# Optimization experiments

Measured on AMD Instinct MI355X. Metric: run time of the kernel, lower is better.

The kernel has to match this reference:

```python
import jax, jax.numpy as jnp
import numpy as np
from jax import lax

# --- constructor constants (init_kwargs) ---
NMS_THRESH = 0.0
NMS_KSIZE = 5
TOP_K = 512
GAUSS_KSIZE = 15
GAUSS_SIGMA = 0.5
LOSS_LAMBDA = 100.0
BORDER = 8  # border width zeroed by filter_border (RF-Net convention)

B, C, H, W = 8, 1, 512, 640


def setup_inputs() -> dict:
    key = jax.random.key(0)
    k1, k2, k3 = jax.random.split(key, 3)
    score1 = jax.random.uniform(k1, (B, C, H, W), dtype=jnp.float32)
    score2 = jax.random.uniform(k2, (B, C, H, W), dtype=jnp.float32)
    # near-identity homographies: small affine perturbation + few-pixel translation
    scale = jnp.array([[0.02, 0.02, 5.0], [0.02, 0.02, 5.0], [1e-5, 1e-5, 0.0]], jnp.float32)
    homo12 = jnp.eye(3, dtype=jnp.float32)[None] + jax.random.normal(k3, (B, 3, 3), jnp.float32) * scale[None]
    return {"score1": score1, "score2": score2, "homo12": homo12}


def filter_border(x, pad=BORDER):
    m = jnp.zeros((x.shape[-2], x.shape[-1]), x.dtype).at[pad:-pad, pad:-pad].set(1.0)
    return x * m


def warp_image(img, homo):
    # Sample img (frame 2) at homo @ p1 for every pixel p1; zero outside. img: B,C,H,W
    b, c, h, w = img.shape
    ys, xs = jnp.meshgrid(jnp.arange(h, dtype=jnp.float32), jnp.arange(w, dtype=jnp.float32), indexing="ij")
    p1 = jnp.stack([xs, ys, jnp.ones_like(xs)], 0).reshape(3, -1)
    p2 = jnp.einsum("bij,jn->bin", homo, p1)
    x2 = (p2[:, 0] / p2[:, 2]).reshape(b, h, w)
    y2 = (p2[:, 1] / p2[:, 2]).reshape(b, h, w)

    x0 = jnp.floor(x2); y0 = jnp.floor(y2)
    x1 = x0 + 1.0; y1 = y0 + 1.0
    wa = (x1 - x2) * (y1 - y2); wb = (x2 - x0) * (y1 - y2)
    wc = (x1 - x2) * (y2 - y0); wd = (x2 - x0) * (y2 - y0)

    bidx = jnp.arange(b)[:, None, None]

    def gather(yc, xc):
        valid = (xc >= 0) & (xc <= w - 1) & (yc >= 0) & (yc <= h - 1)
        xi = jnp.clip(xc, 0, w - 1).astype(jnp.int32)
        yi = jnp.clip(yc, 0, h - 1).astype(jnp.int32)
        g = img[bidx, :, yi, xi]  # B,H,W,C
        return g * valid[..., None].astype(img.dtype)

    out = (wa[..., None] * gather(y0, x0) + wb[..., None] * gather(y0, x1)
           + wc[..., None] * gather(y1, x0) + wd[..., None] * gather(y1, x1))
    return jnp.transpose(out, (0, 3, 1, 2))


def nms(score):
    # zero-pad (matches F.pad + max_pool2d), local-max + threshold mask
    pad = NMS_KSIZE // 2
    p = jnp.pad(score, ((0, 0), (0, 0), (pad, pad), (pad, pad)))
    fmax = lax.reduce_window(p, -jnp.inf, lax.max, (1, 1, NMS_KSIZE, NMS_KSIZE), (1, 1, 1, 1), "VALID")
    mask = (score > NMS_THRESH) & (score == fmax)
    return score * mask.astype(score.dtype)


def select_score_and_keypoints(score):
    s = nms(score)
    b, c, h, w = s.shape
    flat = s.reshape(b * c, h * w)
    vals, idx = lax.top_k(flat, TOP_K)
    sel = jnp.zeros_like(flat).at[jnp.arange(b * c)[:, None], idx].set(vals)
    sel = sel.reshape(b, c, h, w)
    kp = jnp.stack([idx // w, idx % w], -1).reshape(b, c, TOP_K, 2)  # (y, x)
    return sel, kp


def gaussian_filter(x):
    r = GAUSS_KSIZE // 2
    ax = jnp.arange(-r, r + 1, dtype=jnp.float32)
    g1 = jnp.exp(-(ax ** 2) / (2.0 * GAUSS_SIGMA ** 2))
    kern = jnp.outer(g1, g1)  # unnormalized (peak = 1), RF-Net style
    c = x.shape[1]
    k = jnp.broadcast_to(kern[None, None], (c, 1, GAUSS_KSIZE, GAUSS_KSIZE))
    return lax.conv_general_dilated(x, k, (1, 1), "SAME", feature_group_count=c)


def reference(score1, score2, homo12):
    w_score2 = warp_image(score2, homo12)
    s1 = filter_border(score1)
    w2 = filter_border(w_score2)
    w_vis_mask = (warp_image(jnp.ones_like(score2), homo12) > 0).astype(s1.dtype)
    _, kp1 = select_score_and_keypoints(s1)
    gt_score1, _ = select_score_and_keypoints(w2)
    gt_score1 = gaussian_filter(gt_score1)
    norm = w_vis_mask.sum()
    loss = (((s1 - gt_score1) ** 2) * w_vis_mask / norm).sum() * LOSS_LAMBDA
    return loss, kp1
```

## Files before the change

kernel.cpp:

```cpp
#include <hip/hip_runtime.h>

#define NB 8
#define NH 512
#define NW 640
#define NHW (NH*NW)
#define TOPK 512
#define PAD 8
#define NBIN2 256
#define GCAP 4096
#define NTILE 160
#define TSLOT 256

#define TW 64
#define TH 32
#define INH 36
#define INW 72

#define G0 1.0f
#define G1 0.1353352832366127f
#define G2 3.3546262790251185e-4f

#define M_TCNT 0
#define M_THIST 2560
#define M_DENSE 657920
#define M_WCNT 660480
#define M_ACCUM 660488
#define M_DCNT 660496
#define M_WINNERS 660504
#define M_END (M_WINNERS + 8192)

__device__ __forceinline__ float bordered(const float* __restrict__ img, int b, int y, int x) {
  if (y < PAD || y >= NH - PAD || x < PAD || x >= NW - PAD) return 0.f;
  return img[b * NHW + y * NW + x];
}

__device__ __forceinline__ int vbin(float val) {
  int d = 0x3F800000 - (int)__float_as_uint(val);
  if (d < 0) d = 0;
  unsigned int bk = (unsigned int)d >> 14;
  return bk > (NBIN2 - 1) ? (NBIN2 - 1) : (int)bk;
}

__device__ __forceinline__ void corner(const float* __restrict__ img, float cx, float cy,
                                       float wgt, float& acc) {
  float valid = (cx >= 0.f && cx <= (float)(NW - 1) && cy >= 0.f && cy <= (float)(NH - 1)) ? 1.f : 0.f;
  float xc = fminf(fmaxf(cx, 0.f), (float)(NW - 1));
  float yc = fminf(fmaxf(cy, 0.f), (float)(NH - 1));
  int xi = (int)xc, yi = (int)yc;
  acc += wgt * img[yi * NW + xi] * valid;
}

__device__ __forceinline__ float vis_quad(float h0, float h1, float h2, float h3, float h4,
                                          float h5, float h6, float h7, float h8,
                                          float xf, float yf) {
  float X = h0 * xf + h1 * yf + h2;
  float Y = h3 * xf + h4 * yf + h5;
  float Z = h6 * xf + h7 * yf + h8;
  bool ok = ((X + Z) * Z > 0.f) & ((640.f * Z - X) * Z > 0.f)
          & ((Y + Z) * Z > 0.f) & ((512.f * Z - Y) * Z > 0.f);
  return ok ? 1.f : 0.f;
}

__device__ __forceinline__ void vis_parts(float h0, float h1, float h2, float h3, float h4,
                                          float h5, float h6, float h7, float h8,
                                          float xf, float yf, float L[5]) {
  float X = h0 * xf + h1 * yf + h2;
  float Y = h3 * xf + h4 * yf + h5;
  float Z = h6 * xf + h7 * yf + h8;
  L[0] = X + Z; L[1] = 640.f * Z - X; L[2] = Y + Z; L[3] = 512.f * Z - Y; L[4] = Z;
}

__global__ __launch_bounds__(256) void k_nms5(
    const float* __restrict__ score1, const float* __restrict__ score2,
    const float* __restrict__ homo,
    unsigned long long* __restrict__ lists, unsigned int* __restrict__ meta) {
  int bx = blockIdx.x, by = blockIdx.y, b = blockIdx.z;
  int tid = threadIdx.x;
  int t = by * 10 + bx;

  __shared__ float in[INH][INW];
  __shared__ float hmax[INH][TW];
  __shared__ unsigned int s_cnt;
  __shared__ unsigned int s_bh[NBIN2];
  __shared__ float s_wsum[4];
  __shared__ unsigned int s_wcnt[4];

  const float* hm = homo + b * 9;
  float h0 = hm[0], h1 = hm[1], h2 = hm[2];
  float h3 = hm[3], h4 = hm[4], h5 = hm[5];
  float h6 = hm[6], h7 = hm[7], h8 = hm[8];

  int y0t = by * TH, x0t = bx * TW;

  for (int src = 0; src < 2; ++src) {
    if (tid == 0) s_cnt = 0;
    s_bh[tid] = 0;

    if (src == 0) {
      #pragma unroll
      for (int it = 0; it < 3; ++it) {
        int i = it * 256 + tid;
        if (i < INH * 18) {
          int r = i / 18, c4 = i % 18;
          int gy = y0t + r - 2;
          int gx0 = x0t - 4 + c4 * 4;
          float4 v = make_float4(0.f, 0.f, 0.f, 0.f);
          if (gy >= PAD && gy < NH - PAD) {
            const float4* p = (const float4*)(score1 + (size_t)b * NHW + (size_t)gy * NW + gx0);
            float4 raw = *p;
            v.x = (gx0 + 0 >= PAD && gx0 + 0 < NW - PAD) ? raw.x : 0.f;
            v.y = (gx0 + 1 >= PAD && gx0 + 1 < NW - PAD) ? raw.y : 0.f;
            v.z = (gx0 + 2 >= PAD && gx0 + 2 < NW - PAD) ? raw.z : 0.f;
            v.w = (gx0 + 3 >= PAD && gx0 + 3 < NW - PAD) ? raw.w : 0.f;
          }
          *(float4*)&in[r][c4 * 4] = v;
        }
      }
    } else {
      const float* img = score2 + b * NHW;
      #pragma unroll
      for (int it = 0; it < 10; ++it) {
        int i = it * 256 + tid;
        if (i < INH * 68) {
          int r = i / 68, c = i % 68;
          int gy = y0t + r - 2, gx = x0t - 2 + c;
          float v = 0.f;
          if (gy >= PAD && gy < NH - PAD && gx >= PAD && gx < NW - PAD) {
            float xf = (float)gx, yf = (float)gy;
            float X = h0 * xf + h1 * yf + h2;
            float Y = h3 * xf + h4 * yf + h5;
            float Z = h6 * xf + h7 * yf + h8;
            float rz = __builtin_amdgcn_rcpf(Z);
            float x2 = X * rz, y2 = Y * rz;
            float x0f = floorf(x2), y0f = floorf(y2);
            float x1f = x0f + 1.f, y1f = y0f + 1.f;
            float wa = (x1f - x2) * (y1f - y2);
            float wb = (x2 - x0f) * (y1f - y2);
            float wc = (x1f - x2) * (y2 - y0f);
            float wd = (x2 - x0f) * (y2 - y0f);
            float acc = 0.f;
            if (x0f >= 0.f && x1f <= 639.f && y0f >= 0.f && y1f <= 511.f) {
              const float* p = img + (int)y0f * NW + (int)x0f;
              acc = fmaf(wa, p[0], acc);
              acc = fmaf(wb, p[1], acc);
              acc = fmaf(wc, p[NW], acc);
              acc = fmaf(wd, p[NW + 1], acc);
            } else {
              corner(img, x0f, y0f, wa, acc);
              corner(img, x1f, y0f, wb, acc);
              corner(img, x0f, y1f, wc, acc);
              corner(img, x1f, y1f, wd, acc);
            }
            v = acc;
          }
          in[r][c + 2] = v;
        }
      }
    }
    __syncthreads();

    #pragma unroll
    for (int it = 0; it < 9; ++it) {
      int i = it * 256 + tid;
      int r = i >> 6, c = i & 63;
      float m = fmaxf(fmaxf(fmaxf(in[r][c + 2], in[r][c + 3]), fmaxf(in[r][c + 4], in[r][c + 5])),
                      in[r][c + 6]);
      hmax[r][c] = m;
    }
    __syncthreads();

    bool uni = false;
    float vconst = 0.f;
    if (src == 0) {
      float c00[5], c10[5], c01[5], c11[5];
      vis_parts(h0, h1, h2, h3, h4, h5, h6, h7, h8, (float)x0t, (float)y0t, c00);
      vis_parts(h0, h1, h2, h3, h4, h5, h6, h7, h8, (float)(x0t + TW - 1), (float)y0t, c10);
      vis_parts(h0, h1, h2, h3, h4, h5, h6, h7, h8, (float)x0t, (float)(y0t + TH - 1), c01);
      vis_parts(h0, h1, h2, h3, h4, h5, h6, h7, h8, (float)(x0t + TW - 1), (float)(y0t + TH - 1), c11);
      uni = true;
      bool sig[5];
      #pragma unroll
      for (int q = 0; q < 5; ++q) {
        bool allp = (c00[q] > 0.f) & (c10[q] > 0.f) & (c01[q] > 0.f) & (c11[q] > 0.f);
        bool alln = (c00[q] < 0.f) & (c10[q] < 0.f) & (c01[q] < 0.f) & (c11[q] < 0.f);
        uni = uni & (allp | alln);
        sig[q] = allp;
      }
      vconst = (sig[0] == sig[4] && sig[1] == sig[4] && sig[2] == sig[4] && sig[3] == sig[4])
               ? 1.f : 0.f;
    }

    int nsv = 0;
    float sv[8];
    unsigned int si[8];
    float tsum = 0.f;
    int vcnt = 0;
    #pragma unroll
    for (int it = 0; it < (TH * TW) / 256; ++it) {
      int i = it * 256 + tid;
      int r = i >> 6, c = i & 63;
      int gy = y0t + r, gx = x0t + c;
      float val = in[r + 2][c + 4];
      if (src == 0) {
        float v = uni ? vconst
                      : vis_quad(h0, h1, h2, h3, h4, h5, h6, h7, h8, (float)gx, (float)gy);
        tsum += val * val * v;
        vcnt += (v > 0.f) ? 1 : 0;
      }
      if (val > 0.f) {
        float m = fmaxf(fmaxf(fmaxf(hmax[r][c], hmax[r + 1][c]), fmaxf(hmax[r + 2][c], hmax[r + 3][c])),
                        hmax[r + 4][c]);
        if (m == val) {
          sv[nsv] = val;
          si[nsv] = (unsigned int)(gy * NW + gx);
          ++nsv;
        }
      }
    }

    unsigned int local = 0;
    if (nsv > 0) local = atomicAdd(&s_cnt, (unsigned int)nsv);
    #pragma unroll
    for (int j = 0; j < 8; ++j)
      if (j < nsv) atomicAdd(&s_bh[vbin(sv[j])], 1u);

    if (src == 0) {
      for (int m = 1; m < 64; m <<= 1) {
        tsum += __shfl_xor(tsum, m, 64);
        vcnt += __shfl_xor(vcnt, m, 64);
      }
      if ((tid & 63) == 0) { s_wsum[tid >> 6] = tsum; s_wcnt[tid >> 6] = (unsigned int)vcnt; }
    }
    __syncthreads();

    int li = src * NB + b;
    if (tid == 0)
      meta[M_TCNT + li * NTILE + t] = (s_cnt < (unsigned)TSLOT) ? s_cnt : (unsigned)TSLOT;
    meta[M_THIST + (li * NTILE + t) * NBIN2 + tid] = s_bh[tid];
    if (src == 0 && tid == 0) {
      float ts = s_wsum[0] + s_wsum[1] + s_wsum[2] + s_wsum[3];
      unsigned int vc = s_wcnt[0] + s_wcnt[1] + s_wcnt[2] + s_wcnt[3];
      meta[M_DENSE + (b * NTILE + t) * 2 + 0] = __float_as_uint(ts);
      meta[M_DENSE + (b * NTILE + t) * 2 + 1] = vc;
    }
    #pragma unroll
    for (int j = 0; j < 8; ++j) {
      if (j < nsv && local + (unsigned)j < (unsigned)TSLOT) {
        unsigned long long key = ((unsigned long long)__float_as_uint(sv[j]) << 32)
                               | (unsigned long long)(~si[j]);
        lists[(size_t)li * (NTILE * TSLOT) + t * TSLOT + local + j] = key;
      }
    }
    __syncthreads();
  }
}

#define NT 1024
__global__ __launch_bounds__(NT) void k_topk9(
    const unsigned long long* __restrict__ lists, unsigned int* __restrict__ meta,
    float* __restrict__ out) {
  int li = blockIdx.x;
  int src = li >> 3, b = li & 7;
  int tid = threadIdx.x;

  __shared__ unsigned long long sbuf[GCAP];
  __shared__ unsigned long long srt[TOPK];
  __shared__ unsigned int scnt[NTILE];
  __shared__ unsigned int s_bc[NBIN2];
  __shared__ int s_sbb;
  __shared__ unsigned int s_nsel;

  if (tid < NTILE) scnt[tid] = meta[M_TCNT + li * NTILE + tid];
  if (tid < NBIN2) s_bc[tid] = 0;
  if (tid == 0) { s_nsel = 0; s_sbb = NBIN2 - 1; }
  if (li == 0 && tid == 0) {
    ((unsigned long long*)(meta + M_ACCUM))[0] = 0ULL;
    meta[M_DCNT] = 0u;
  }
  __syncthreads();

  for (int i = tid; i < NTILE * NBIN2; i += NT)
    atomicAdd(&s_bc[i & (NBIN2 - 1)], meta[M_THIST + li * (NTILE * NBIN2) + i]);
  __syncthreads();

  for (int off = 1; off < NBIN2; off <<= 1) {
    unsigned int v = 0;
    if (tid < NBIN2 && tid >= off) v = s_bc[tid - off];
    __syncthreads();
    if (tid < NBIN2) s_bc[tid] += v;
    __syncthreads();
  }
  unsigned int N = s_bc[NBIN2 - 1];
  unsigned int want = (N < TOPK) ? N : TOPK;
  if (tid < NBIN2 && want > 0) {
    unsigned int cum = s_bc[tid];
    unsigned int prev = (tid == 0) ? 0u : s_bc[tid - 1];
    if (cum >= want && prev < want) s_sbb = tid;
  }
  __syncthreads();
  int sbb = s_sbb;

  const unsigned long long* list = lists + (size_t)li * (NTILE * TSLOT);
  int lane = tid & 63;
  for (unsigned int s = tid; s < NTILE * TSLOT; s += NT) {
    unsigned int t = s >> 8, j = s & 255u;
    bool pred = (j < scnt[t]);
    unsigned long long k = 0ULL;
    if (pred) {
      k = list[s];
      float v = __uint_as_float((unsigned int)(k >> 32));
      pred = (vbin(v) <= sbb);
    }
    unsigned long long mask = __ballot(pred);
    if (mask) {
      int leader = __ffsll((long long)mask) - 1;
      unsigned int cnt = (unsigned int)__popcll(mask);
      unsigned int bp = 0;
      if (lane == leader) bp = atomicAdd(&s_nsel, cnt);
      bp = __shfl(bp, leader, 64);
      if (pred) {
        unsigned int pos = bp + (unsigned int)__popcll(mask & ((1ULL << lane) - 1ULL));
        if (pos < GCAP) sbuf[pos] = k;
      }
    }
  }
  __syncthreads();
  unsigned int total = s_nsel; if (total > GCAP) total = GCAP;

  for (unsigned int i = tid; i < total; i += NT) {
    unsigned long long key = sbuf[i];
    unsigned int rank = 0;
    for (unsigned int j = 0; j < total; ++j)
      rank += (sbuf[j] > key) ? 1u : 0u;
    if (rank < TOPK) srt[rank] = key;
  }
  for (unsigned int i = total + tid; i < TOPK; i += NT) srt[i] = 0ULL;
  __syncthreads();

  if (src == 0) {
    for (int r = tid; r < TOPK; r += NT) {
      unsigned long long k = srt[r];
      unsigned int idx = (k == 0ULL) ? 0u : ~(unsigned int)(k & 0xFFFFFFFFULL);
      int yy = (int)(idx / NW), xx = (int)(idx % NW);
      out[1 + ((b * TOPK) + r) * 2 + 0] = (float)yy;
      out[1 + ((b * TOPK) + r) * 2 + 1] = (float)xx;
    }
  } else {
    unsigned int nw = (total < TOPK) ? total : TOPK;
    unsigned long long* winners = (unsigned long long*)(meta + M_WINNERS);
    for (unsigned int i = tid; i < nw; i += NT) {
      unsigned long long k = srt[i];
      unsigned int idx = ~(unsigned int)(k & 0xFFFFFFFFULL);
      unsigned int rank = 0;
      for (unsigned int j = 0; j < nw; ++j) {
        unsigned int idxj = ~(unsigned int)(srt[j] & 0xFFFFFFFFULL);
        rank += (idxj < idx) ? 1u : 0u;
      }
      winners[b * TOPK + rank] = ((unsigned long long)idx << 32) | (k >> 32);
    }
    for (unsigned int i = nw + tid; i < TOPK; i += NT) winners[b * TOPK + i] = ~0ULL;
    if (tid == 0) meta[M_WCNT + b] = nw;
  }
}

__global__ __launch_bounds__(256) void k_gt2(
    const float* __restrict__ score1, const float* __restrict__ homo,
    unsigned int* __restrict__ meta, float* __restrict__ out) {
  int b = blockIdx.y;
  int tid = threadIdx.x;
  __shared__ unsigned long long w[TOPK];
  __shared__ float s_red[4];
  __shared__ double s_dd[256];
  __shared__ unsigned long long s_cnt64[256];

  unsigned long long* accum = (unsigned long long*)(meta + M_ACCUM);
  const unsigned long long* winners = (const unsigned long long*)(meta + M_WINNERS);
  unsigned int nw = meta[M_WCNT + b];
  for (int i = tid; i < TOPK; i += 256)
    w[i] = (i < (int)nw) ? winners[b * TOPK + i] : ~0ULL;
  __syncthreads();

  const float* hm = homo + b * 9;
  float h0 = hm[0], h1 = hm[1], h2 = hm[2];
  float h3 = hm[3], h4 = hm[4], h5 = hm[5];
  float h6 = hm[6], h7 = hm[7], h8 = hm[8];

  const float gw5[5] = {G2, G1, G0, G1, G2};
  unsigned int r = blockIdx.x * 256u + (unsigned int)tid;
  unsigned int i = r / 25u, k = r % 25u;
  float term = 0.f;
  if (i < nw) {
    unsigned long long wk = w[i];
    unsigned int idx = (unsigned int)(wk >> 32);
    int y = (int)(idx / NW), x = (int)(idx % NW);
    int py = y + (int)(k / 5u) - 2, px = x + (int)(k % 5u) - 2;

    float gt = 0.f;
    unsigned int firstIdx = 0xFFFFFFFFu;
    #pragma unroll
    for (int dr = -2; dr <= 2; ++dr) {
      int ry = py + dr;
      unsigned int lo = (unsigned int)(ry * NW + px - 2);
      unsigned int hi = (unsigned int)(ry * NW + px + 2);
      unsigned long long lokey = ((unsigned long long)lo << 32);
      int a = 0, e = TOPK;
      while (a < e) { int m = (a + e) >> 1; if (w[m] < lokey) a = m + 1; else e = m; }
      for (int j = a; j < TOPK; ++j) {
        unsigned long long c = w[j];
        unsigned int cidx = (unsigned int)(c >> 32);
        if (cidx > hi) break;
        float cval = __uint_as_float((unsigned int)(c & 0xFFFFFFFFULL));
        int cx = (int)(cidx % NW);
        gt += cval * gw5[dr + 2] * gw5[cx - px + 2];
        if (firstIdx == 0xFFFFFFFFu) firstIdx = cidx;
      }
    }
    if (firstIdx == idx) {
      float s1 = bordered(score1, b, py, px);
      float v = vis_quad(h0, h1, h2, h3, h4, h5, h6, h7, h8, (float)px, (float)py);
      term = (gt - 2.f * s1) * gt * v;
    }
  }

  for (int m = 1; m < 64; m <<= 1) term += __shfl_xor(term, m, 64);
  if ((tid & 63) == 0) s_red[tid >> 6] = term;

  if (blockIdx.x == 0 && blockIdx.y == 0) {
    double dsum = 0.0;
    unsigned long long dn = 0;
    for (int i2 = tid; i2 < NB * NTILE; i2 += 256) {
      dsum += (double)__uint_as_float(meta[M_DENSE + 2 * i2]);
      dn += (unsigned long long)meta[M_DENSE + 2 * i2 + 1];
    }
    s_dd[tid] = dsum;
    s_cnt64[tid] = dn;
    __syncthreads();
    for (int s = 128; s > 0; s >>= 1) {
      if (tid < s) { s_dd[tid] += s_dd[tid + s]; s_cnt64[tid] += s_cnt64[tid + s]; }
      __syncthreads();
    }
    if (tid == 0) {
      accum[2] = (unsigned long long)__double_as_longlong(s_dd[0]);
      accum[3] = s_cnt64[0];
    }
  }
  __syncthreads();

  if (tid == 0) {
    float bsum = s_red[0] + s_red[1] + s_red[2] + s_red[3];
    long long fp = (long long)((double)bsum * 4294967296.0);
    atomicAdd(&accum[0], (unsigned long long)fp);
    __threadfence();
    unsigned int old = atomicAdd(meta + M_DCNT, 1u);
    if (old == gridDim.x * gridDim.y - 1u) {
      unsigned long long corr = atomicAdd(&accum[0], 0ULL);
      unsigned long long dbits = atomicAdd(&accum[2], 0ULL);
      unsigned long long nv = atomicAdd(&accum[3], 0ULL);
      double dense = __longlong_as_double((long long)dbits);
      double corrd = (double)(long long)corr / 4294967296.0;
      out[0] = (float)(100.0 * (dense + corrd) / (double)nv);
    }
  }
}

extern "C" void kernel_launch(void* const* d_in, const int* in_sizes, int n_in,
                              void* d_out, int out_size, void* d_ws, size_t ws_size,
                              hipStream_t stream) {
  const float* score1 = (const float*)d_in[0];
  const float* score2 = (const float*)d_in[1];
  const float* homo   = (const float*)d_in[2];
  float* out = (float*)d_out;

  unsigned long long* lists = (unsigned long long*)d_ws;
  unsigned int* meta = (unsigned int*)(lists + (size_t)16 * NTILE * TSLOT);

  size_t required = (size_t)16 * NTILE * TSLOT * 8 + (size_t)M_END * 4;
  if (ws_size < required) return;

  dim3 gnms(NW / TW, NH / TH, NB);
  k_nms5<<<gnms, 256, 0, stream>>>(score1, score2, homo, lists, meta);
  k_topk9<<<16, NT, 0, stream>>>(lists, meta, out);
  dim3 ggt((TOPK * 25) / 256, NB);
  k_gt2<<<ggt, 256, 0, stream>>>(score1, homo, meta, out);
}
```

Before: 98.01 us.

## Split top-k into parallel gather and rank kernels with global histogram atomics

Per-tile histograms are now merged into a global per-image histogram with atomics in the NMS kernel, instead of writing 160x256 entries that the top-k kernel re-reduced. The candidate gather is spread over 128 blocks (8 chunks per list) appending to a global candidate buffer, and a separate 16-block kernel performs the rank sort. This targets the serial 16-block top-k stage, at the cost of an extra memset, an extra kernel launch, and global atomics. Moving ACCUM/DCNT zeroing into the memset also changes where that initialization happens.

```diff
diff --git a/kernel.cpp b/kernel.cpp
--- a/kernel.cpp
+++ b/kernel.cpp
@@ -10,6 +10,8 @@
 #define GCAP 4096
 #define NTILE 160
 #define TSLOT 256
+#define NCHUNK 8
+#define TPC 20
 
 #define TW 64
 #define TH 32
@@ -20,13 +22,16 @@
 #define G1 0.1353352832366127f
 #define G2 3.3546262790251185e-4f
 
-#define M_TCNT 0
-#define M_THIST 2560
-#define M_DENSE 657920
-#define M_WCNT 660480
-#define M_ACCUM 660488
-#define M_DCNT 660496
-#define M_WINNERS 660504
+#define M_BINS 0
+#define M_NCAND 4096
+#define M_TCNT 4112
+#define M_DENSE 6672
+#define M_WCNT 9232
+#define M_ACCUM 9240
+#define M_DCNT 9248
+#define M_ZERO_END 9252
+#define M_CAND 9256
+#define M_WINNERS 140328
 #define M_END (M_WINNERS + 8192)
 
 __device__ __forceinline__ float bordered(const float* __restrict__ img, int b, int y, int x) {
@@ -236,7 +241,8 @@
     int li = src * NB + b;
     if (tid == 0)
       meta[M_TCNT + li * NTILE + t] = (s_cnt < (unsigned)TSLOT) ? s_cnt : (unsigned)TSLOT;
-    meta[M_THIST + (li * NTILE + t) * NBIN2 + tid] = s_bh[tid];
+    if (s_bh[tid] > 0)
+      atomicAdd(&meta[M_BINS + li * NBIN2 + tid], s_bh[tid]);
     if (src == 0 && tid == 0) {
       float ts = s_wsum[0] + s_wsum[1] + s_wsum[2] + s_wsum[3];
       unsigned int vc = s_wcnt[0] + s_wcnt[1] + s_wcnt[2] + s_wcnt[3];
@@ -255,32 +261,18 @@
   }
 }
 
-#define NT 1024
-__global__ __launch_bounds__(NT) void k_topk9(
-    const unsigned long long* __restrict__ lists, unsigned int* __restrict__ meta,
-    float* __restrict__ out) {
-  int li = blockIdx.x;
-  int src = li >> 3, b = li & 7;
+__global__ __launch_bounds__(1024) void k_gath(
+    const unsigned long long* __restrict__ lists, unsigned int* __restrict__ meta) {
+  int li = blockIdx.x >> 3;
+  int c  = blockIdx.x & 7;
   int tid = threadIdx.x;
-
-  __shared__ unsigned long long sbuf[GCAP];
-  __shared__ unsigned long long srt[TOPK];
-  __shared__ unsigned int scnt[NTILE];
   __shared__ unsigned int s_bc[NBIN2];
+  __shared__ unsigned int scnt[TPC];
   __shared__ int s_sbb;
-  __shared__ unsigned int s_nsel;
-
-  if (tid < NTILE) scnt[tid] = meta[M_TCNT + li * NTILE + tid];
-  if (tid < NBIN2) s_bc[tid] = 0;
-  if (tid == 0) { s_nsel = 0; s_sbb = NBIN2 - 1; }
-  if (li == 0 && tid == 0) {
-    ((unsigned long long*)(meta + M_ACCUM))[0] = 0ULL;
-    meta[M_DCNT] = 0u;
-  }
-  __syncthreads();
-
-  for (int i = tid; i < NTILE * NBIN2; i += NT)
-    atomicAdd(&s_bc[i & (NBIN2 - 1)], meta[M_THIST + li * (NTILE * NBIN2) + i]);
+
+  if (tid < NBIN2) s_bc[tid] = meta[M_BINS + li * NBIN2 + tid];
+  if (tid < TPC) scnt[tid] = meta[M_TCNT + li * NTILE + c * TPC + tid];
+  if (tid == 0) s_sbb = NBIN2 - 1;
   __syncthreads();
 
   for (int off = 1; off < NBIN2; off <<= 1) {
@@ -298,47 +290,63 @@
     if (cum >= want && prev < want) s_sbb = tid;
   }
   __syncthreads();
-  int sbb = s_sbb;
-
-  const unsigned long long* list = lists + (size_t)li * (NTILE * TSLOT);
+  int bb = s_sbb;
+
+  const unsigned long long* list = lists + (size_t)li * (NTILE * TSLOT)
+                                         + (size_t)c * (TPC * TSLOT);
+  unsigned long long* cand = (unsigned long long*)(meta + M_CAND) + (size_t)li * GCAP;
   int lane = tid & 63;
-  for (unsigned int s = tid; s < NTILE * TSLOT; s += NT) {
+  #pragma unroll
+  for (int it = 0; it < (TPC * TSLOT) / 1024; ++it) {
+    unsigned int s = it * 1024 + tid;
     unsigned int t = s >> 8, j = s & 255u;
     bool pred = (j < scnt[t]);
     unsigned long long k = 0ULL;
     if (pred) {
       k = list[s];
       float v = __uint_as_float((unsigned int)(k >> 32));
-      pred = (vbin(v) <= sbb);
+      pred = (vbin(v) <= bb);
     }
     unsigned long long mask = __ballot(pred);
     if (mask) {
       int leader = __ffsll((long long)mask) - 1;
       unsigned int cnt = (unsigned int)__popcll(mask);
       unsigned int bp = 0;
-      if (lane == leader) bp = atomicAdd(&s_nsel, cnt);
+      if (lane == leader) bp = atomicAdd(&meta[M_NCAND + li], cnt);
       bp = __shfl(bp, leader, 64);
       if (pred) {
         unsigned int pos = bp + (unsigned int)__popcll(mask & ((1ULL << lane) - 1ULL));
-        if (pos < GCAP) sbuf[pos] = k;
-      }
-    }
-  }
-  __syncthreads();
-  unsigned int total = s_nsel; if (total > GCAP) total = GCAP;
-
-  for (unsigned int i = tid; i < total; i += NT) {
+        if (pos < GCAP) cand[pos] = k;
+      }
+    }
+  }
+}
+
+__global__ __launch_bounds__(1024) void k_rank(
+    unsigned int* __restrict__ meta, float* __restrict__ out) {
+  int li = blockIdx.x;
+  int src = li >> 3, b = li & 7;
+  int tid = threadIdx.x;
+  __shared__ unsigned long long sbuf[GCAP];
+  __shared__ unsigned long long srt[TOPK];
+
+  unsigned int n = meta[M_NCAND + li]; if (n > GCAP) n = GCAP;
+  const unsigned long long* cand = (const unsigned long long*)(meta + M_CAND) + (size_t)li * GCAP;
+  for (unsigned int i = tid; i < n; i += 1024) sbuf[i] = cand[i];
+  __syncthreads();
+
+  for (unsigned int i = tid; i < n; i += 1024) {
     unsigned long long key = sbuf[i];
     unsigned int rank = 0;
-    for (unsigned int j = 0; j < total; ++j)
+    for (unsigned int j = 0; j < n; ++j)
       rank += (sbuf[j] > key) ? 1u : 0u;
     if (rank < TOPK) srt[rank] = key;
   }
-  for (unsigned int i = total + tid; i < TOPK; i += NT) srt[i] = 0ULL;
+  for (unsigned int i = n + tid; i < TOPK; i += 1024) srt[i] = 0ULL;
   __syncthreads();
 
   if (src == 0) {
-    for (int r = tid; r < TOPK; r += NT) {
+    for (int r = tid; r < TOPK; r += 1024) {
       unsigned long long k = srt[r];
       unsigned int idx = (k == 0ULL) ? 0u : ~(unsigned int)(k & 0xFFFFFFFFULL);
       int yy = (int)(idx / NW), xx = (int)(idx % NW);
@@ -346,9 +354,9 @@
       out[1 + ((b * TOPK) + r) * 2 + 1] = (float)xx;
     }
   } else {
-    unsigned int nw = (total < TOPK) ? total : TOPK;
+    unsigned int nw = (n < TOPK) ? n : TOPK;
     unsigned long long* winners = (unsigned long long*)(meta + M_WINNERS);
-    for (unsigned int i = tid; i < nw; i += NT) {
+    for (unsigned int i = tid; i < nw; i += 1024) {
       unsigned long long k = srt[i];
       unsigned int idx = ~(unsigned int)(k & 0xFFFFFFFFULL);
       unsigned int rank = 0;
@@ -358,7 +366,7 @@
       }
       winners[b * TOPK + rank] = ((unsigned long long)idx << 32) | (k >> 32);
     }
-    for (unsigned int i = nw + tid; i < TOPK; i += NT) winners[b * TOPK + i] = ~0ULL;
+    for (unsigned int i = nw + tid; i < TOPK; i += 1024) winners[b * TOPK + i] = ~0ULL;
     if (tid == 0) meta[M_WCNT + b] = nw;
   }
 }
@@ -477,9 +485,12 @@
   size_t required = (size_t)16 * NTILE * TSLOT * 8 + (size_t)M_END * 4;
   if (ws_size < required) return;
 
+  hipMemsetAsync(meta, 0, (size_t)M_ZERO_END * 4, stream);
+
   dim3 gnms(NW / TW, NH / TH, NB);
   k_nms5<<<gnms, 256, 0, stream>>>(score1, score2, homo, lists, meta);
-  k_topk9<<<16, NT, 0, stream>>>(lists, meta, out);
+  k_gath<<<128, 1024, 0, stream>>>(lists, meta);
+  k_rank<<<16, 1024, 0, stream>>>(meta, out);
   dim3 ggt((TOPK * 25) / 256, NB);
   k_gt2<<<ggt, 256, 0, stream>>>(score1, homo, meta, out);
 }
```

New measurement: 116.1 us. 1.18x slower.
